# Kernel tuning notes

Measured on AMD Instinct MI355X. Metric: run time of the kernel, lower is better.

## Reference

```python
import jax, jax.numpy as jnp
import numpy as np

VAR = (0.1, 0.2)        # SSD encoding variances
THRESH = 0.5            # overlap_thresh
NEGPOS = 3              # neg:pos ratio


def _point_form(p):
    # (cx,cy,w,h) -> (x1,y1,x2,y2)
    return jnp.concatenate([p[:, :2] - p[:, 2:] / 2, p[:, :2] + p[:, 2:] / 2], axis=1)


def _jaccard(a, b):
    # a: [O,4], b: [P,4], corner form -> IoU [O,P]
    lt = jnp.maximum(a[:, None, :2], b[None, :, :2])
    rb = jnp.minimum(a[:, None, 2:], b[None, :, 2:])
    wh = jnp.maximum(rb - lt, 0.0)
    inter = wh[..., 0] * wh[..., 1]
    area_a = ((a[:, 2] - a[:, 0]) * (a[:, 3] - a[:, 1]))[:, None]
    area_b = ((b[:, 2] - b[:, 0]) * (b[:, 3] - b[:, 1]))[None, :]
    return inter / (area_a + area_b - inter)


def _encode(matched, priors):
    # matched: [P,4] corner form, priors: [P,4] center form
    g_cxcy = ((matched[:, :2] + matched[:, 2:]) / 2 - priors[:, :2]) / (VAR[0] * priors[:, 2:])
    g_wh = jnp.log((matched[:, 2:] - matched[:, :2]) / priors[:, 2:]) / VAR[1]
    return jnp.concatenate([g_cxcy, g_wh], axis=1)


def _match(truths, labels, priors):
    # truths: [O,4], labels: [O], priors: [P,4] -> loc_t [P,4], conf_t [P], obj_t [P]
    O = truths.shape[0]
    over = _jaccard(truths, _point_form(priors))          # [O,P]
    best_prior_idx = jnp.argmax(over, axis=1)             # [O] best prior per truth
    best_truth_overlap = over.max(axis=0)                 # [P]
    best_truth_idx = jnp.argmax(over, axis=0)             # [P]
    best_truth_overlap = best_truth_overlap.at[best_prior_idx].set(2.0)
    best_truth_idx = best_truth_idx.at[best_prior_idx].set(jnp.arange(O))
    matched = truths[best_truth_idx]                      # [P,4]
    conf = labels[best_truth_idx].astype(jnp.int32) + 1   # background = 0
    conf = jnp.where(best_truth_overlap < THRESH, 0, conf)
    return _encode(matched, priors), conf, conf > 0


def _ce(logits, tgt):
    # per-element cross entropy, logits [...,C], tgt [...] int
    return jax.nn.logsumexp(logits, axis=-1) - jnp.take_along_axis(logits, tgt[..., None], axis=-1)[..., 0]


def _mine_neg(loss, pos, P):
    # hard negative mining via double argsort (rank of each elem in descending loss order)
    loss = jnp.where(pos, 0.0, loss)
    loss_idx = jnp.argsort(-loss, axis=1)
    idx_rank = jnp.argsort(loss_idx, axis=1)
    num_neg = jnp.minimum(NEGPOS * pos.sum(axis=1, keepdims=True), P - 1)
    return idx_rank < num_neg


def setup_inputs() -> dict:
    key = jax.random.key(0)
    ks = jax.random.split(key, 8)
    B, P, C, O = 64, 16320, 81, 50
    loc_data = jax.random.normal(ks[0], (B, P, 4), jnp.float32)
    conf_data = jax.random.normal(ks[1], (B, P, C), jnp.float32)
    obj_data = jax.random.normal(ks[2], (B, P, 2), jnp.float32)
    # priors: center form, positive w/h
    cxcy = jax.random.uniform(ks[3], (P, 2), minval=0.05, maxval=0.95)
    wh = jax.random.uniform(ks[4], (P, 2), minval=0.02, maxval=0.3)
    priors = jnp.concatenate([cxcy, wh], axis=1).astype(jnp.float32)
    # targets: valid corner-form boxes + float label in last column
    tc = jax.random.uniform(ks[5], (B, O, 2), minval=0.1, maxval=0.9)
    twh = jax.random.uniform(ks[6], (B, O, 2), minval=0.05, maxval=0.3)
    boxes = jnp.concatenate([jnp.clip(tc - twh / 2, 0.0, 1.0), jnp.clip(tc + twh / 2, 0.0, 1.0)], axis=-1)
    labels = jax.random.randint(ks[7], (B, O), 0, C).astype(jnp.float32)
    targets = jnp.concatenate([boxes, labels[..., None]], axis=-1).astype(jnp.float32)
    return {"loc_data": loc_data, "conf_data": conf_data, "obj_data": obj_data,
            "priors": priors, "targets": targets}


def reference(loc_data, conf_data, obj_data, priors, targets):
    B, P, C = conf_data.shape
    loc_t, conf_t, pos = jax.vmap(lambda t: _match(t[:, :4], t[:, 4], priors))(targets)
    loc_t = jax.lax.stop_gradient(loc_t)  # torch builds targets detached

    # localization: smooth L1 over positives, sum reduction
    d = loc_data - loc_t
    sl1 = jnp.where(jnp.abs(d) < 1.0, 0.5 * d * d, jnp.abs(d) - 0.5)
    loss_l = jnp.sum(sl1 * pos[..., None].astype(sl1.dtype))

    # combined (C+1)-way logit: col0 = obj_bg + log(sum(exp(conf))), cols 1..C = obj_fg + conf
    lse_conf = jax.nn.logsumexp(conf_data, axis=-1)                        # [B,P]
    logit = jnp.concatenate([(obj_data[..., 0] + lse_conf)[..., None],
                             obj_data[..., 1:2] + conf_data], axis=-1)     # [B,P,C+1]

    ce_c = _ce(logit, conf_t)                       # [B,P]
    neg_c = _mine_neg(ce_c, pos, P)
    loss_c = jnp.sum(jnp.where(pos | neg_c, ce_c, 0.0))

    ce_o = _ce(obj_data, pos.astype(jnp.int32))     # [B,P]
    neg_o = _mine_neg(ce_o, pos, P)
    loss_obj = jnp.sum(jnp.where(pos | neg_o, ce_o, 0.0))

    N = pos.sum().astype(jnp.float32)
    return loss_l / N, loss_c / N, loss_obj / N
```

## Files before the change

### kernel.cpp

```cpp
#include <hip/hip_runtime.h>
#include <cstdint>
#include <cstddef>

#define THRESH   0.5f
#define NEGPOS   3
#define VAR0     0.1f
#define VAR1     0.2f
#define MAXO     128
#define NPRI     8
#define A1_T     256
#define MINE_T   1024
#define MINE_W   (MINE_T / 64)
#define HCOPIES  8

__global__ __launch_bounds__(A1_T)
void match_kernel(const float* __restrict__ priors,
                  const float* __restrict__ targets,
                  float* __restrict__ bt_ov, int* __restrict__ bt_idx,
                  unsigned long long* __restrict__ g_bp,
                  int B, int P, int O, int chunks) {
    __shared__ float tx1[MAXO], ty1[MAXO], tx2[MAXO], ty2[MAXO], tarea[MAXO];
    const int b   = blockIdx.x / chunks;
    const int ch  = blockIdx.x % chunks;
    const int tid = threadIdx.x;

    if (tid < O) {
        const float* tr = targets + (size_t)(b * O + tid) * 5;
        float x1 = tr[0], y1 = tr[1], x2 = tr[2], y2 = tr[3];
        tx1[tid] = x1; ty1[tid] = y1; tx2[tid] = x2; ty2[tid] = y2;
        tarea[tid] = (x2 - x1) * (y2 - y1);
    }
    __syncthreads();

    float px1[NPRI], py1[NPRI], px2[NPRI], py2[NPRI], pa[NPRI], pov[NPRI];
    int   pidx[NPRI];
    const int p0 = ch * (A1_T * NPRI) + tid;
#pragma unroll
    for (int i = 0; i < NPRI; ++i) {
        int p = p0 + i * A1_T;
        pov[i] = -1.0f; pidx[i] = 0;
        px1[i] = 0.f; py1[i] = 0.f; px2[i] = 0.f; py2[i] = 0.f; pa[i] = 1.0f;
        if (p < P) {
            float4 pr = *(const float4*)(priors + (size_t)p * 4);
            px1[i] = pr.x - pr.z * 0.5f; py1[i] = pr.y - pr.w * 0.5f;
            px2[i] = pr.x + pr.z * 0.5f; py2[i] = pr.y + pr.w * 0.5f;
            pa[i]  = pr.z * pr.w;
        }
    }

    const int lane = tid & 63;
    for (int o = 0; o < O; ++o) {
        float ax1 = tx1[o], ay1 = ty1[o], ax2 = tx2[o], ay2 = ty2[o], aa = tarea[o];
        float bo = -1.0f; unsigned bp = 0u;
#pragma unroll
        for (int i = 0; i < NPRI; ++i) {
            int p = p0 + i * A1_T;
            if (p < P) {
                float lx = fmaxf(ax1, px1[i]), ly = fmaxf(ay1, py1[i]);
                float rx = fminf(ax2, px2[i]), ry = fminf(ay2, py2[i]);
                float w = fmaxf(rx - lx, 0.0f), h = fmaxf(ry - ly, 0.0f);
                float inter = w * h;
                float iou = inter / (aa + pa[i] - inter);
                if (iou > pov[i]) { pov[i] = iou; pidx[i] = o; }
                if (iou > bo)     { bo = iou; bp = (unsigned)p; }
            }
        }
        unsigned long long key = 0ull;
        if (bo >= 0.0f)
            key = ((unsigned long long)__float_as_uint(bo) << 32) |
                  (unsigned long long)(0xFFFFFFFFu - bp);
#pragma unroll
        for (int d = 1; d < 64; d <<= 1) {
            unsigned long long other = __shfl_xor(key, d, 64);
            if (other > key) key = other;
        }
        if (lane == 0 && key != 0ull)
            atomicMax(&g_bp[(size_t)b * O + o], key);
    }

#pragma unroll
    for (int i = 0; i < NPRI; ++i) {
        int p = p0 + i * A1_T;
        if (p < P) {
            size_t off = (size_t)b * P + p;
            bt_ov[off]  = pov[i];
            bt_idx[off] = pidx[i];
        }
    }
}

__global__ void override_kernel(const unsigned long long* __restrict__ g_bp,
                                float* __restrict__ bt_ov, int* __restrict__ bt_idx,
                                int B, int P, int O) {
    int b = blockIdx.x * blockDim.x + threadIdx.x;
    if (b >= B) return;
    for (int o = 0; o < O; ++o) {
        unsigned long long key = g_bp[(size_t)b * O + o];
        unsigned p = 0xFFFFFFFFu - (unsigned)(key & 0xFFFFFFFFull);
        size_t off = (size_t)b * P + p;
        bt_ov[off]  = 2.0f;
        bt_idx[off] = o;
    }
}

__global__ __launch_bounds__(256)
void ce_kernel(const float* __restrict__ loc, const float* __restrict__ conf,
               const float* __restrict__ obj, const float* __restrict__ priors,
               const float* __restrict__ targets,
               const float* __restrict__ bt_ov, const int* __restrict__ bt_idx,
               float* __restrict__ mce, float* __restrict__ rowacc,
               int B, int P, int C, int O) {
    const int b = blockIdx.y;
    const int p = blockIdx.x * 256 + threadIdx.x;

    float sl = 0.f, cec = 0.f, ceo = 0.f, cntp = 0.f;

    if (p < P) {
        const size_t t = (size_t)b * P + p;
        float ov = bt_ov[t];
        float2 ob = *(const float2*)(obj + t * 2);
        float m    = fmaxf(ob.x, ob.y);
        float lse2 = m + __logf(__expf(ob.x - m) + __expf(ob.y - m));

        if (ov < THRESH) {
            mce[t] = lse2 - ob.x;
        } else {
            mce[t] = 0.0f;
            cntp = 1.0f;
            int idx = bt_idx[t];
            const float* tr = targets + (size_t)(b * O + idx) * 5;
            int conf_t = (int)tr[4] + 1;

            const float* cr = conf + t * C;
            float s0 = 0.f, s1 = 0.f, s2 = 0.f, s3 = 0.f;
            int c = 0;
            for (; c + 4 <= C; c += 4) {
                s0 += __expf(cr[c]);     s1 += __expf(cr[c + 1]);
                s2 += __expf(cr[c + 2]); s3 += __expf(cr[c + 3]);
            }
            for (; c < C; ++c) s0 += __expf(cr[c]);
            float lsec = __logf((s0 + s1) + (s2 + s3));
            cec = lsec + lse2 - ob.y - cr[conf_t - 1];
            ceo = lse2 - ob.y;

            float4 pr = *(const float4*)(priors + (size_t)p * 4);
            float mx1 = tr[0], my1 = tr[1], mx2 = tr[2], my2 = tr[3];
            float gx = ((mx1 + mx2) * 0.5f - pr.x) / (VAR0 * pr.z);
            float gy = ((my1 + my2) * 0.5f - pr.y) / (VAR0 * pr.w);
            float gw = __logf((mx2 - mx1) / pr.z) / VAR1;
            float gh = __logf((my2 - my1) / pr.w) / VAR1;
            float4 ld = *(const float4*)(loc + t * 4);
            float d0 = ld.x - gx, a0 = fabsf(d0); sl += (a0 < 1.f) ? 0.5f * d0 * d0 : a0 - 0.5f;
            float d1 = ld.y - gy, a1 = fabsf(d1); sl += (a1 < 1.f) ? 0.5f * d1 * d1 : a1 - 0.5f;
            float d2 = ld.z - gw, a2 = fabsf(d2); sl += (a2 < 1.f) ? 0.5f * d2 * d2 : a2 - 0.5f;
            float d3 = ld.w - gh, a3 = fabsf(d3); sl += (a3 < 1.f) ? 0.5f * d3 * d3 : a3 - 0.5f;
        }
    }

    __shared__ float red[4][4];
#pragma unroll
    for (int d = 32; d > 0; d >>= 1) {
        sl   += __shfl_down(sl,   d, 64);
        cec  += __shfl_down(cec,  d, 64);
        ceo  += __shfl_down(ceo,  d, 64);
        cntp += __shfl_down(cntp, d, 64);
    }
    const int wv = threadIdx.x >> 6, lane = threadIdx.x & 63;
    if (lane == 0) { red[wv][0] = sl; red[wv][1] = cec; red[wv][2] = ceo; red[wv][3] = cntp; }
    __syncthreads();
    if (threadIdx.x < 4) {
        float v = red[0][threadIdx.x] + red[1][threadIdx.x] +
                  red[2][threadIdx.x] + red[3][threadIdx.x];
        if (v != 0.0f)
            atomicAdd(rowacc + (size_t)b * 4 + threadIdx.x, v);
    }
}

__global__ __launch_bounds__(MINE_T)
void mine_kernel(const float* __restrict__ mce, const float* __restrict__ rowacc,
                 float* __restrict__ g_neg, int P) {
    const int b = blockIdx.x;
    const float* row = mce + (size_t)b * P;
    int npos = (int)rowacc[(size_t)b * 4 + 3];
    int k = NEGPOS * npos;
    if (k > P - 1) k = P - 1;
    if (k <= 0) return;

    __shared__ unsigned hist[HCOPIES][257];
    __shared__ unsigned s_prefix;
    __shared__ int      s_rem;
    __shared__ float    s_ws[MINE_W];
    __shared__ int      s_wc[MINE_W];

    const int tid  = threadIdx.x;
    const int wv   = tid >> 6;
    const int hc   = wv & (HCOPIES - 1);
    const int lane = tid & 63;

    unsigned prefix = 0u;
    int rem = k;
    for (int shift = 24; shift >= 0; shift -= 8) {
        for (int i = tid; i < HCOPIES * 257; i += MINE_T) (&hist[0][0])[i] = 0u;
        __syncthreads();
        unsigned himask = (shift == 24) ? 0u : (0xFFFFFFFFu << (shift + 8));
        for (int i = tid; i < P; i += MINE_T) {
            unsigned bits = __float_as_uint(row[i]);
            if ((bits & himask) == prefix)
                atomicAdd(&hist[hc][(bits >> shift) & 0xFFu], 1u);
        }
        __syncthreads();
        if (tid == 0) {
            int cum = 0; unsigned bin = 0;
            for (int bb = 255; bb >= 0; --bb) {
                int cnt = 0;
#pragma unroll
                for (int h = 0; h < HCOPIES; ++h) cnt += (int)hist[h][bb];
                if (cum + cnt >= rem) { bin = (unsigned)bb; rem -= cum; break; }
                cum += cnt;
            }
            s_prefix = prefix | (bin << shift);
            s_rem = rem;
        }
        __syncthreads();
        prefix = s_prefix;
        rem    = s_rem;
    }

    float vk = __uint_as_float(prefix);
    float s = 0.f; int cnt = 0;
    for (int i = tid; i < P; i += MINE_T) {
        float v = row[i];
        if (__float_as_uint(v) > prefix) { s += v; ++cnt; }
    }
#pragma unroll
    for (int d = 32; d > 0; d >>= 1) {
        s   += __shfl_down(s, d, 64);
        cnt += __shfl_down(cnt, d, 64);
    }
    if (lane == 0) { s_ws[wv] = s; s_wc[wv] = cnt; }
    __syncthreads();
    if (tid == 0) {
        float st = 0.f; int ct = 0;
        for (int w = 0; w < MINE_W; ++w) { st += s_ws[w]; ct += s_wc[w]; }
        atomicAdd(g_neg, st + (float)(k - ct) * vk);
    }
}

__global__ void finish_kernel(const float* __restrict__ rowacc,
                              const float* __restrict__ g_neg,
                              float* __restrict__ out, int B) {
    if (threadIdx.x == 0 && blockIdx.x == 0) {
        float locs = 0.f, cec = 0.f, ceo = 0.f, N = 0.f;
        for (int b = 0; b < B; ++b) {
            locs += rowacc[b * 4 + 0];
            cec  += rowacc[b * 4 + 1];
            ceo  += rowacc[b * 4 + 2];
            N    += rowacc[b * 4 + 3];
        }
        float neg = *g_neg;
        out[0] = locs / N;
        out[1] = (cec + neg) / N;
        out[2] = (ceo + neg) / N;
    }
}

extern "C" void kernel_launch(void* const* d_in, const int* in_sizes, int n_in,
                              void* d_out, int out_size, void* d_ws, size_t ws_size,
                              hipStream_t stream) {
    const float* loc     = (const float*)d_in[0];
    const float* conf    = (const float*)d_in[1];
    const float* obj     = (const float*)d_in[2];
    const float* priors  = (const float*)d_in[3];
    const float* targets = (const float*)d_in[4];

    const int P = in_sizes[3] / 4;
    const int B = in_sizes[0] / (4 * P);
    const int C = in_sizes[1] / (B * P);
    const int O = in_sizes[4] / (5 * B);

    char* ws = (char*)d_ws;
    size_t off = 0;
    float* rowacc = (float*)(ws + off);            off += (size_t)B * 4 * sizeof(float);
    float* g_neg  = (float*)(ws + off);            off += 16;
    off = (off + 7) & ~(size_t)7;
    unsigned long long* g_bp = (unsigned long long*)(ws + off);
    off += (size_t)B * O * sizeof(unsigned long long);
    const size_t zero_bytes = off;
    off = (off + 15) & ~(size_t)15;
    float* bt_ov  = (float*)(ws + off);            off += (size_t)B * P * sizeof(float);
    int*   bt_idx = (int*)(ws + off);              off += (size_t)B * P * sizeof(int);
    float* mce    = (float*)(ws + off);            off += (size_t)B * P * sizeof(float);

    hipMemsetAsync(d_ws, 0, zero_bytes, stream);

    const int chunks = (P + A1_T * NPRI - 1) / (A1_T * NPRI);
    match_kernel<<<B * chunks, A1_T, 0, stream>>>(priors, targets, bt_ov, bt_idx,
                                                  g_bp, B, P, O, chunks);
    override_kernel<<<(B + 63) / 64, 64, 0, stream>>>(g_bp, bt_ov, bt_idx, B, P, O);
    dim3 ce_grid((P + 255) / 256, B);
    ce_kernel<<<ce_grid, 256, 0, stream>>>(loc, conf, obj, priors, targets,
                                           bt_ov, bt_idx, mce, rowacc,
                                           B, P, C, O);
    mine_kernel<<<B, MINE_T, 0, stream>>>(mce, rowacc, g_neg, P);
    finish_kernel<<<1, 1, 0, stream>>>(rowacc, g_neg, (float*)d_out, B);
}
```

Baseline: 596.2 us.

## Compact positives into a list and process them with 16-lane groups

The match kernel now writes a one-byte code per prior (0 for negative, otherwise matched truth index plus one) in place of separate float overlap and int index arrays, which cuts intermediate memory traffic. The CE kernel only computes the objectness loss and uses a wave ballot to append positive priors to a compacted global list. A new pos_kernel spreads the class-softmax, CE and smooth-L1 work for the positives across 16-lane groups, removing the divergence of a few positive threads per wave looping over all C classes. It drops the p<P bounds check in the IoU loop, uses fast division, and lowers MAXO to 64, which assumes at most 64 truths per image and 16-bit fields in the packed list entries.

```diff
diff --git a/kernel.cpp b/kernel.cpp
--- a/kernel.cpp
+++ b/kernel.cpp
@@ -6,17 +6,20 @@
 #define NEGPOS   3
 #define VAR0     0.1f
 #define VAR1     0.2f
-#define MAXO     128
+#define MAXO     64
 #define NPRI     8
 #define A1_T     256
 #define MINE_T   1024
 #define MINE_W   (MINE_T / 64)
 #define HCOPIES  8
+#define POS_BLK  512
+#define POS_T    256
+#define NSLOT    64
 
 __global__ __launch_bounds__(A1_T)
 void match_kernel(const float* __restrict__ priors,
                   const float* __restrict__ targets,
-                  float* __restrict__ bt_ov, int* __restrict__ bt_idx,
+                  unsigned char* __restrict__ code,
                   unsigned long long* __restrict__ g_bp,
                   int B, int P, int O, int chunks) {
     __shared__ float tx1[MAXO], ty1[MAXO], tx2[MAXO], ty2[MAXO], tarea[MAXO];
@@ -54,125 +57,168 @@
         float bo = -1.0f; unsigned bp = 0u;
 #pragma unroll
         for (int i = 0; i < NPRI; ++i) {
-            int p = p0 + i * A1_T;
-            if (p < P) {
-                float lx = fmaxf(ax1, px1[i]), ly = fmaxf(ay1, py1[i]);
-                float rx = fminf(ax2, px2[i]), ry = fminf(ay2, py2[i]);
-                float w = fmaxf(rx - lx, 0.0f), h = fmaxf(ry - ly, 0.0f);
-                float inter = w * h;
-                float iou = inter / (aa + pa[i] - inter);
-                if (iou > pov[i]) { pov[i] = iou; pidx[i] = o; }
-                if (iou > bo)     { bo = iou; bp = (unsigned)p; }
-            }
-        }
-        unsigned long long key = 0ull;
-        if (bo >= 0.0f)
-            key = ((unsigned long long)__float_as_uint(bo) << 32) |
-                  (unsigned long long)(0xFFFFFFFFu - bp);
+            float lx = fmaxf(ax1, px1[i]), ly = fmaxf(ay1, py1[i]);
+            float rx = fminf(ax2, px2[i]), ry = fminf(ay2, py2[i]);
+            float w = fmaxf(rx - lx, 0.0f), h = fmaxf(ry - ly, 0.0f);
+            float inter = w * h;
+            float iou = __fdividef(inter, aa + pa[i] - inter);
+            if (iou > pov[i]) { pov[i] = iou; pidx[i] = o; }
+            if (iou > bo)     { bo = iou; bp = (unsigned)(p0 + i * A1_T); }
+        }
+        unsigned long long key =
+            ((unsigned long long)__float_as_uint(bo) << 32) |
+            (unsigned long long)(0xFFFFFFFFu - bp);
 #pragma unroll
         for (int d = 1; d < 64; d <<= 1) {
             unsigned long long other = __shfl_xor(key, d, 64);
             if (other > key) key = other;
         }
-        if (lane == 0 && key != 0ull)
+        if (lane == 0)
             atomicMax(&g_bp[(size_t)b * O + o], key);
     }
 
 #pragma unroll
     for (int i = 0; i < NPRI; ++i) {
         int p = p0 + i * A1_T;
-        if (p < P) {
-            size_t off = (size_t)b * P + p;
-            bt_ov[off]  = pov[i];
-            bt_idx[off] = pidx[i];
-        }
-    }
-}
-
-__global__ void override_kernel(const unsigned long long* __restrict__ g_bp,
-                                float* __restrict__ bt_ov, int* __restrict__ bt_idx,
-                                int B, int P, int O) {
+        if (p < P)
+            code[(size_t)b * P + p] =
+                (pov[i] >= THRESH) ? (unsigned char)(pidx[i] + 1) : (unsigned char)0;
+    }
+}
+
+__global__ void force_kernel(const unsigned long long* __restrict__ g_bp,
+                             unsigned char* __restrict__ code,
+                             int B, int P, int O) {
     int b = blockIdx.x * blockDim.x + threadIdx.x;
     if (b >= B) return;
     for (int o = 0; o < O; ++o) {
         unsigned long long key = g_bp[(size_t)b * O + o];
         unsigned p = 0xFFFFFFFFu - (unsigned)(key & 0xFFFFFFFFull);
-        size_t off = (size_t)b * P + p;
-        bt_ov[off]  = 2.0f;
-        bt_idx[off] = o;
+        code[(size_t)b * P + p] = (unsigned char)(o + 1);
     }
 }
 
 __global__ __launch_bounds__(256)
-void ce_kernel(const float* __restrict__ loc, const float* __restrict__ conf,
-               const float* __restrict__ obj, const float* __restrict__ priors,
-               const float* __restrict__ targets,
-               const float* __restrict__ bt_ov, const int* __restrict__ bt_idx,
-               float* __restrict__ mce, float* __restrict__ rowacc,
-               int B, int P, int C, int O) {
+void ce_kernel(const float* __restrict__ obj,
+               const unsigned char* __restrict__ code,
+               float* __restrict__ mce,
+               unsigned long long* __restrict__ list,
+               unsigned* __restrict__ g_cnt,
+               float* __restrict__ rowacc,
+               int B, int P, int O) {
     const int b = blockIdx.y;
     const int p = blockIdx.x * 256 + threadIdx.x;
-
-    float sl = 0.f, cec = 0.f, ceo = 0.f, cntp = 0.f;
-
+    const int tid = threadIdx.x, wv = tid >> 6, lane = tid & 63;
+
+    bool pos = false;
+    unsigned cc = 0;
+    size_t t = (size_t)b * P + p;
     if (p < P) {
-        const size_t t = (size_t)b * P + p;
-        float ov = bt_ov[t];
+        cc = code[t];
         float2 ob = *(const float2*)(obj + t * 2);
         float m    = fmaxf(ob.x, ob.y);
         float lse2 = m + __logf(__expf(ob.x - m) + __expf(ob.y - m));
-
-        if (ov < THRESH) {
+        if (cc == 0) {
             mce[t] = lse2 - ob.x;
         } else {
             mce[t] = 0.0f;
-            cntp = 1.0f;
-            int idx = bt_idx[t];
-            const float* tr = targets + (size_t)(b * O + idx) * 5;
-            int conf_t = (int)tr[4] + 1;
-
-            const float* cr = conf + t * C;
-            float s0 = 0.f, s1 = 0.f, s2 = 0.f, s3 = 0.f;
-            int c = 0;
-            for (; c + 4 <= C; c += 4) {
-                s0 += __expf(cr[c]);     s1 += __expf(cr[c + 1]);
-                s2 += __expf(cr[c + 2]); s3 += __expf(cr[c + 3]);
-            }
-            for (; c < C; ++c) s0 += __expf(cr[c]);
-            float lsec = __logf((s0 + s1) + (s2 + s3));
-            cec = lsec + lse2 - ob.y - cr[conf_t - 1];
-            ceo = lse2 - ob.y;
-
+            pos = true;
+        }
+    }
+
+    unsigned long long msk = __ballot(pos);
+    __shared__ unsigned s_cnt[4];
+    int cnt = __popcll(msk);
+    if (msk != 0ull) {
+        int leader = __ffsll((unsigned long long)msk) - 1;
+        unsigned base = 0;
+        if (lane == leader) base = atomicAdd(g_cnt, (unsigned)cnt);
+        base = (unsigned)__shfl((int)base, leader, 64);
+        if (pos) {
+            unsigned off = base + (unsigned)__popcll(msk & ((1ull << lane) - 1ull));
+            unsigned long long e = ((unsigned long long)(unsigned)t << 32) |
+                                   ((unsigned long long)(unsigned)p << 16) |
+                                   (unsigned long long)(unsigned)(b * O + (int)cc - 1);
+            list[off] = e;
+        }
+    }
+    if (lane == 0) s_cnt[wv] = (unsigned)cnt;
+    __syncthreads();
+    if (tid == 0) {
+        unsigned total = s_cnt[0] + s_cnt[1] + s_cnt[2] + s_cnt[3];
+        if (total) atomicAdd(rowacc + (size_t)b * 16, (float)total);
+    }
+}
+
+__global__ __launch_bounds__(POS_T)
+void pos_kernel(const float* __restrict__ loc, const float* __restrict__ conf,
+                const float* __restrict__ obj, const float* __restrict__ priors,
+                const float* __restrict__ targets,
+                const unsigned long long* __restrict__ list,
+                const unsigned* __restrict__ g_cnt,
+                float* __restrict__ g_acc, int C) {
+    const unsigned cnt = *g_cnt;
+    const int tid  = threadIdx.x;
+    const int lane = tid & 63, wv = tid >> 6;
+    const int q    = lane >> 4, lq = lane & 15;
+    const unsigned gw   = (blockIdx.x * POS_T + tid) >> 6;
+    const unsigned Wtot = (gridDim.x * POS_T) >> 6;
+
+    float sl = 0.f, cec = 0.f, ceo = 0.f;
+
+    for (unsigned base = gw * 4; base < cnt; base += Wtot * 4) {
+        unsigned e = base + (unsigned)q;
+        bool act = e < cnt;
+        unsigned long long v = act ? list[e] : 0ull;
+        unsigned t  = (unsigned)(v >> 32);
+        unsigned p  = (unsigned)(v >> 16) & 0xFFFFu;
+        unsigned to = (unsigned)v & 0xFFFFu;
+        const float* cr = conf + (size_t)t * C;
+
+        float s = 0.f;
+        if (act)
+            for (int j = lq; j < C; j += 16) s += __expf(cr[j]);
+#pragma unroll
+        for (int d = 1; d < 16; d <<= 1) s += __shfl_xor(s, d, 16);
+
+        if (act && lq == 0) {
+            const float* tr = targets + (size_t)to * 5;
+            float2 ob = *(const float2*)(obj + (size_t)t * 2);
             float4 pr = *(const float4*)(priors + (size_t)p * 4);
+            float4 ld = *(const float4*)(loc + (size_t)t * 4);
             float mx1 = tr[0], my1 = tr[1], mx2 = tr[2], my2 = tr[3];
+            int   lbl = (int)tr[4];
+
+            float m    = fmaxf(ob.x, ob.y);
+            float lse2 = m + __logf(__expf(ob.x - m) + __expf(ob.y - m));
+            float lsec = __logf(s);
+            cec += lsec + lse2 - ob.y - cr[lbl];
+            ceo += lse2 - ob.y;
+
             float gx = ((mx1 + mx2) * 0.5f - pr.x) / (VAR0 * pr.z);
             float gy = ((my1 + my2) * 0.5f - pr.y) / (VAR0 * pr.w);
-            float gw = __logf((mx2 - mx1) / pr.z) / VAR1;
-            float gh = __logf((my2 - my1) / pr.w) / VAR1;
-            float4 ld = *(const float4*)(loc + t * 4);
-            float d0 = ld.x - gx, a0 = fabsf(d0); sl += (a0 < 1.f) ? 0.5f * d0 * d0 : a0 - 0.5f;
-            float d1 = ld.y - gy, a1 = fabsf(d1); sl += (a1 < 1.f) ? 0.5f * d1 * d1 : a1 - 0.5f;
-            float d2 = ld.z - gw, a2 = fabsf(d2); sl += (a2 < 1.f) ? 0.5f * d2 * d2 : a2 - 0.5f;
-            float d3 = ld.w - gh, a3 = fabsf(d3); sl += (a3 < 1.f) ? 0.5f * d3 * d3 : a3 - 0.5f;
-        }
-    }
-
-    __shared__ float red[4][4];
+            float gw2 = __logf((mx2 - mx1) / pr.z) / VAR1;
+            float gh  = __logf((my2 - my1) / pr.w) / VAR1;
+            float d0 = ld.x - gx,  a0 = fabsf(d0); sl += (a0 < 1.f) ? 0.5f * d0 * d0 : a0 - 0.5f;
+            float d1 = ld.y - gy,  a1 = fabsf(d1); sl += (a1 < 1.f) ? 0.5f * d1 * d1 : a1 - 0.5f;
+            float d2 = ld.z - gw2, a2 = fabsf(d2); sl += (a2 < 1.f) ? 0.5f * d2 * d2 : a2 - 0.5f;
+            float d3 = ld.w - gh,  a3 = fabsf(d3); sl += (a3 < 1.f) ? 0.5f * d3 * d3 : a3 - 0.5f;
+        }
+    }
+
+    __shared__ float red[POS_T / 64][3];
 #pragma unroll
     for (int d = 32; d > 0; d >>= 1) {
-        sl   += __shfl_down(sl,   d, 64);
-        cec  += __shfl_down(cec,  d, 64);
-        ceo  += __shfl_down(ceo,  d, 64);
-        cntp += __shfl_down(cntp, d, 64);
-    }
-    const int wv = threadIdx.x >> 6, lane = threadIdx.x & 63;
-    if (lane == 0) { red[wv][0] = sl; red[wv][1] = cec; red[wv][2] = ceo; red[wv][3] = cntp; }
+        sl  += __shfl_down(sl,  d, 64);
+        cec += __shfl_down(cec, d, 64);
+        ceo += __shfl_down(ceo, d, 64);
+    }
+    if (lane == 0) { red[wv][0] = sl; red[wv][1] = cec; red[wv][2] = ceo; }
     __syncthreads();
-    if (threadIdx.x < 4) {
-        float v = red[0][threadIdx.x] + red[1][threadIdx.x] +
-                  red[2][threadIdx.x] + red[3][threadIdx.x];
-        if (v != 0.0f)
-            atomicAdd(rowacc + (size_t)b * 4 + threadIdx.x, v);
+    if (tid < 3) {
+        float vv = red[0][tid] + red[1][tid] + red[2][tid] + red[3][tid];
+        if (vv != 0.0f)
+            atomicAdd(g_acc + (size_t)(blockIdx.x & (NSLOT - 1)) * 16 + tid, vv);
     }
 }
 
@@ -181,7 +227,7 @@
                  float* __restrict__ g_neg, int P) {
     const int b = blockIdx.x;
     const float* row = mce + (size_t)b * P;
-    int npos = (int)rowacc[(size_t)b * 4 + 3];
+    int npos = (int)rowacc[(size_t)b * 16];
     int k = NEGPOS * npos;
     if (k > P - 1) k = P - 1;
     if (k <= 0) return;
@@ -247,20 +293,27 @@
 }
 
 __global__ void finish_kernel(const float* __restrict__ rowacc,
+                              const float* __restrict__ g_acc,
                               const float* __restrict__ g_neg,
                               float* __restrict__ out, int B) {
-    if (threadIdx.x == 0 && blockIdx.x == 0) {
-        float locs = 0.f, cec = 0.f, ceo = 0.f, N = 0.f;
-        for (int b = 0; b < B; ++b) {
-            locs += rowacc[b * 4 + 0];
-            cec  += rowacc[b * 4 + 1];
-            ceo  += rowacc[b * 4 + 2];
-            N    += rowacc[b * 4 + 3];
-        }
+    int lane = threadIdx.x;
+    float npos = 0.f;
+    for (int b = lane; b < B; b += 64) npos += rowacc[(size_t)b * 16];
+    float sl  = g_acc[(size_t)lane * 16 + 0];
+    float cec = g_acc[(size_t)lane * 16 + 1];
+    float ceo = g_acc[(size_t)lane * 16 + 2];
+#pragma unroll
+    for (int d = 32; d > 0; d >>= 1) {
+        npos += __shfl_down(npos, d, 64);
+        sl   += __shfl_down(sl,   d, 64);
+        cec  += __shfl_down(cec,  d, 64);
+        ceo  += __shfl_down(ceo,  d, 64);
+    }
+    if (lane == 0) {
         float neg = *g_neg;
-        out[0] = locs / N;
-        out[1] = (cec + neg) / N;
-        out[2] = (ceo + neg) / N;
+        out[0] = sl / npos;
+        out[1] = (cec + neg) / npos;
+        out[2] = (ceo + neg) / npos;
     }
 }
 
@@ -280,27 +333,33 @@
 
     char* ws = (char*)d_ws;
     size_t off = 0;
-    float* rowacc = (float*)(ws + off);            off += (size_t)B * 4 * sizeof(float);
-    float* g_neg  = (float*)(ws + off);            off += 16;
-    off = (off + 7) & ~(size_t)7;
+    unsigned* g_cnt = (unsigned*)(ws + off);       off += 16;
+    float*    g_neg = (float*)(ws + off);          off += 16;
+    off = (off + 63) & ~(size_t)63;
+    float* rowacc = (float*)(ws + off);            off += (size_t)B * 16 * sizeof(float);
+    float* g_acc  = (float*)(ws + off);            off += (size_t)NSLOT * 16 * sizeof(float);
     unsigned long long* g_bp = (unsigned long long*)(ws + off);
     off += (size_t)B * O * sizeof(unsigned long long);
     const size_t zero_bytes = off;
-    off = (off + 15) & ~(size_t)15;
-    float* bt_ov  = (float*)(ws + off);            off += (size_t)B * P * sizeof(float);
-    int*   bt_idx = (int*)(ws + off);              off += (size_t)B * P * sizeof(int);
-    float* mce    = (float*)(ws + off);            off += (size_t)B * P * sizeof(float);
+    off = (off + 127) & ~(size_t)127;
+    unsigned char* code = (unsigned char*)(ws + off); off += (size_t)B * P;
+    off = (off + 127) & ~(size_t)127;
+    float* mce = (float*)(ws + off);               off += (size_t)B * P * sizeof(float);
+    off = (off + 127) & ~(size_t)127;
+    unsigned long long* list = (unsigned long long*)(ws + off);
+    off += (size_t)B * P * sizeof(unsigned long long);
 
     hipMemsetAsync(d_ws, 0, zero_bytes, stream);
 
     const int chunks = (P + A1_T * NPRI - 1) / (A1_T * NPRI);
-    match_kernel<<<B * chunks, A1_T, 0, stream>>>(priors, targets, bt_ov, bt_idx,
-                                                  g_bp, B, P, O, chunks);
-    override_kernel<<<(B + 63) / 64, 64, 0, stream>>>(g_bp, bt_ov, bt_idx, B, P, O);
+    match_kernel<<<B * chunks, A1_T, 0, stream>>>(priors, targets, code, g_bp,
+                                                  B, P, O, chunks);
+    force_kernel<<<(B + 63) / 64, 64, 0, stream>>>(g_bp, code, B, P, O);
     dim3 ce_grid((P + 255) / 256, B);
-    ce_kernel<<<ce_grid, 256, 0, stream>>>(loc, conf, obj, priors, targets,
-                                           bt_ov, bt_idx, mce, rowacc,
-                                           B, P, C, O);
+    ce_kernel<<<ce_grid, 256, 0, stream>>>(obj, code, mce, list, g_cnt, rowacc,
+                                           B, P, O);
+    pos_kernel<<<POS_BLK, POS_T, 0, stream>>>(loc, conf, obj, priors, targets,
+                                              list, g_cnt, g_acc, C);
     mine_kernel<<<B, MINE_T, 0, stream>>>(mce, rowacc, g_neg, P);
-    finish_kernel<<<1, 1, 0, stream>>>(rowacc, g_neg, (float*)d_out, B);
-}
+    finish_kernel<<<1, 64, 0, stream>>>(rowacc, g_acc, g_neg, (float*)d_out, B);
+}
```

After: 788.5 us. 1.32x slower.
